# Kernel optimization log

Hardware: AMD Instinct MI355X
Metric: run time of the kernel (lower is better)

The kernel has to match this reference:

```python
import jax, jax.numpy as jnp
import numpy as np

N_NODES = 50000
N_EDGES = 1600000
IN_FEATS = 256
NUM_HEADS = 4
OUT_FEATS = 32
NEG_SLOPE = 0.2


def setup_inputs() -> dict:
    key = jax.random.key(0)
    k_feat, k_src, k_dst, k_w, k_al, k_ar = jax.random.split(key, 6)
    feat = jax.random.normal(k_feat, (N_NODES, IN_FEATS), dtype=jnp.float32)
    src = jax.random.randint(k_src, (N_EDGES,), 0, N_NODES, dtype=jnp.int32)
    dst = jax.random.randint(k_dst, (N_EDGES,), 0, N_NODES, dtype=jnp.int32)
    # Glorot/xavier-like scales
    w_scale = np.sqrt(2.0 / (IN_FEATS + NUM_HEADS * OUT_FEATS)).astype(np.float32)
    a_scale = np.sqrt(2.0 / (1 + OUT_FEATS)).astype(np.float32)
    W_fc = jax.random.normal(k_w, (NUM_HEADS * OUT_FEATS, IN_FEATS), dtype=jnp.float32) * w_scale
    attn_l = jax.random.normal(k_al, (1, NUM_HEADS, OUT_FEATS), dtype=jnp.float32) * a_scale
    attn_r = jax.random.normal(k_ar, (1, NUM_HEADS, OUT_FEATS), dtype=jnp.float32) * a_scale
    bias = jnp.zeros((NUM_HEADS * OUT_FEATS,), dtype=jnp.float32)
    return {"feat": feat, "W_fc": W_fc, "attn_l": attn_l, "attn_r": attn_r,
            "bias": bias, "src": src, "dst": dst}


def reference(feat, W_fc, attn_l, attn_r, bias, src, dst):
    N = feat.shape[0]
    H, F = NUM_HEADS, OUT_FEATS
    # dense projection: [N, H, F]
    h = (feat @ W_fc.T).reshape(N, H, F)
    # per-node attention logits: [N, H]
    el = (h * attn_l).sum(axis=-1)
    er = (h * attn_r).sum(axis=-1)
    # u_add_v edge score + leaky relu: [E, H]
    e = el[src] + er[dst]
    e = jnp.where(e >= 0, e, NEG_SLOPE * e)
    # segment softmax over destination nodes
    m = jax.ops.segment_max(e, dst, num_segments=N)          # [N, H]
    m = jnp.where(jnp.isfinite(m), m, 0.0)                   # guard 0-in-degree
    e_exp = jnp.exp(e - m[dst])                              # [E, H]
    denom = jax.ops.segment_sum(e_exp, dst, num_segments=N)  # [N, H]
    denom = jnp.where(denom > 0, denom, 1.0)
    a = e_exp / denom[dst]                                   # [E, H]
    # weighted message aggregation: [N, H, F]
    msg = h[src] * a[:, :, None]                             # [E, H, F]
    out = jax.ops.segment_sum(msg, dst, num_segments=N)
    out = out + bias.reshape(1, H, F)
    return out
```

## Files before the change

kernel.cpp:

```cpp
#include <hip/hip_runtime.h>

typedef __attribute__((ext_vector_type(8))) short bf16x8;
typedef __attribute__((ext_vector_type(4))) float f32x4;

#define IN_F 256
#define HF 128
#define NHEADS 4
#define NEG 0.2f

#define RB 256
#define NBP 200
#define CHUNK 6400
#define ITPT 25
#define BCAP 10000

__device__ __forceinline__ unsigned short f2bf(float x) {
    unsigned u = __float_as_uint(x);
    unsigned r = (u + 0x7FFFu + ((u >> 16) & 1u)) >> 16;
    return (unsigned short)r;
}
__device__ __forceinline__ float bf2f(unsigned short b) {
    return __uint_as_float((unsigned)b << 16);
}

__global__ __launch_bounds__(256) void wconv_kernel(const float* __restrict__ W,
                                                    unsigned short* __restrict__ Wb) {
    int i = (blockIdx.x * 256 + threadIdx.x) * 4;
    if (i < HF * IN_F) {
        float4 v = *(const float4*)&W[i];
        ushort4 o;
        o.x = f2bf(v.x); o.y = f2bf(v.y); o.z = f2bf(v.z); o.w = f2bf(v.w);
        *(ushort4*)&Wb[i] = o;
    }
}

__global__ __launch_bounds__(256) void gemm_kernel(
    const float* __restrict__ feat, const unsigned short* __restrict__ Wb,
    const float* __restrict__ al, const float* __restrict__ ar,
    unsigned short* __restrict__ hb, float* __restrict__ el, float* __restrict__ er,
    int N)
{
    __shared__ char smem[64 * 256 * 2];
    const int t = threadIdx.x;
    const int lane = t & 63;
    const int wid = t >> 6;
    const int n0 = blockIdx.x * 64;
    const int lr = lane & 15;
    const int lkO = (lane >> 4) * 8;

    bf16x8 b[2][8];
#pragma unroll
    for (int nj = 0; nj < 2; nj++)
#pragma unroll
        for (int ks = 0; ks < 8; ks++)
            b[nj][ks] = *(const bf16x8*)&Wb[(size_t)(wid * 32 + nj * 16 + lr) * IN_F + ks * 32 + lkO];

    const float4 z4 = make_float4(0.f, 0.f, 0.f, 0.f);
#pragma unroll
    for (int i = 0; i < 16; i++) {
        int flat = i * 1024 + t * 4;
        int row = flat >> 8;
        int col = flat & 255;
        int n = n0 + row;
        float4 v = (n < N) ? *(const float4*)&feat[(size_t)n * IN_F + col] : z4;
        ushort4 s;
        s.x = f2bf(v.x); s.y = f2bf(v.y); s.z = f2bf(v.z); s.w = f2bf(v.w);
        int byte = (row * 512 + col * 2) ^ ((row & 7) << 4);
        *(ushort4*)(smem + byte) = s;
    }
    __syncthreads();

    f32x4 acc[4][2];
#pragma unroll
    for (int mi = 0; mi < 4; mi++)
#pragma unroll
        for (int nj = 0; nj < 2; nj++) acc[mi][nj] = (f32x4){0.f, 0.f, 0.f, 0.f};

#pragma unroll
    for (int mi = 0; mi < 4; mi++) {
        const int r = mi * 16 + lr;
#pragma unroll
        for (int ks = 0; ks < 8; ks++) {
            int byte = (r * 512 + (ks * 32 + lkO) * 2) ^ ((r & 7) << 4);
            bf16x8 a = *(const bf16x8*)(smem + byte);
            acc[mi][0] = __builtin_amdgcn_mfma_f32_16x16x32_bf16(a, b[0][ks], acc[mi][0], 0, 0, 0);
            acc[mi][1] = __builtin_amdgcn_mfma_f32_16x16x32_bf16(a, b[1][ks], acc[mi][1], 0, 0, 0);
        }
    }

    float alc0 = al[wid * 32 + lr],      arc0 = ar[wid * 32 + lr];
    float alc1 = al[wid * 32 + 16 + lr], arc1 = ar[wid * 32 + 16 + lr];
    const int crow = (lane >> 4) * 4;
#pragma unroll
    for (int mi = 0; mi < 4; mi++)
#pragma unroll
        for (int j = 0; j < 4; j++) {
            int n = n0 + mi * 16 + crow + j;
            if (n < N) {
                hb[(size_t)n * HF + wid * 32 + lr]      = f2bf(acc[mi][0][j]);
                hb[(size_t)n * HF + wid * 32 + 16 + lr] = f2bf(acc[mi][1][j]);
            }
            float e = acc[mi][0][j] * alc0 + acc[mi][1][j] * alc1;
            float r2 = acc[mi][0][j] * arc0 + acc[mi][1][j] * arc1;
#pragma unroll
            for (int off = 1; off < 16; off <<= 1) {
                e += __shfl_xor(e, off);
                r2 += __shfl_xor(r2, off);
            }
            if (lr == 0 && n < N) {
                el[n * 4 + wid] = e;
                er[n * 4 + wid] = r2;
            }
        }
}

__global__ __launch_bounds__(256) void part_kernel(const int* __restrict__ src,
                                                   const int* __restrict__ dst,
                                                   int* __restrict__ ebuf,
                                                   int* __restrict__ cntArr,
                                                   int* __restrict__ ofsArr, int E) {
    __shared__ int cnt[256];
    __shared__ int sc[256];
    __shared__ int cur[256];
    __shared__ int stage[CHUNK];
    const int blk = blockIdx.x, t = threadIdx.x;
    const int eb = blk * CHUNK;
    cnt[t] = 0;
    __syncthreads();

    int bkt[ITPT], ent[ITPT];
#pragma unroll
    for (int i = 0; i < ITPT; i++) {
        int idx = eb + i * 256 + t;
        int b = NBP - 1, e = 0;
        if (idx < E) {
            int d = dst[idx];
            int s = src[idx];
            b = d >> 8;
            e = s | ((d & 255) << 24);
        }
        bkt[i] = b;
        ent[i] = e;
        atomicAdd(&cnt[b], 1);
    }
    __syncthreads();
    int orig = cnt[t];
    sc[t] = orig;
    __syncthreads();
    for (int off = 1; off < 256; off <<= 1) {
        int v = (t >= off) ? sc[t - off] : 0;
        __syncthreads();
        sc[t] += v;
        __syncthreads();
    }
    int excl = sc[t] - orig;
    if (t < NBP) {
        cntArr[blk * NBP + t] = orig;
        ofsArr[blk * NBP + t] = excl;
    }
    cur[t] = excl;
    __syncthreads();
#pragma unroll
    for (int i = 0; i < ITPT; i++) {
        int pos = atomicAdd(&cur[bkt[i]], 1);
        stage[pos] = ent[i];
    }
    __syncthreads();
#pragma unroll
    for (int i = 0; i < ITPT; i++) {
        int idx = i * 256 + t;
        ebuf[eb + idx] = stage[idx];
    }
}

__global__ __launch_bounds__(256) void bscan_kernel(const int* __restrict__ cntArr,
                                                    int* __restrict__ bucketStart, int nblk) {
    __shared__ int sums[256];
    const int t = threadIdx.x;
    int s = 0;
    if (t < NBP)
        for (int blk = 0; blk < nblk; blk++) s += cntArr[blk * NBP + t];
    sums[t] = s;
    __syncthreads();
    for (int off = 1; off < 256; off <<= 1) {
        int v = (t >= off) ? sums[t - off] : 0;
        __syncthreads();
        sums[t] += v;
        __syncthreads();
    }
    if (t < NBP) bucketStart[t] = sums[t] - s;
}

__global__ __launch_bounds__(256) void bsort_kernel(const int* __restrict__ ebuf,
                                                    const int* __restrict__ cntArr,
                                                    const int* __restrict__ ofsArr,
                                                    const int* __restrict__ bucketStart,
                                                    int* __restrict__ rowStart,
                                                    int* __restrict__ esrc,
                                                    int nblk, int N, int E) {
    __shared__ int lcnt[256];
    __shared__ int lsc[256];
    __shared__ int lcur[256];
    __shared__ int sorted[BCAP];
    const int b = blockIdx.x, t = threadIdx.x;
    const int gbase = bucketStart[b];
    lcnt[t] = 0;
    __syncthreads();

    int rbase = 0, rlen = 0;
    if (t < nblk) {
        rbase = t * CHUNK + ofsArr[t * NBP + b];
        rlen = cntArr[t * NBP + b];
    }
    int i = 0;
    for (; i + 3 < rlen; i += 4) {
        unsigned e0 = (unsigned)ebuf[rbase + i];
        unsigned e1 = (unsigned)ebuf[rbase + i + 1];
        unsigned e2 = (unsigned)ebuf[rbase + i + 2];
        unsigned e3 = (unsigned)ebuf[rbase + i + 3];
        atomicAdd(&lcnt[e0 >> 24], 1);
        atomicAdd(&lcnt[e1 >> 24], 1);
        atomicAdd(&lcnt[e2 >> 24], 1);
        atomicAdd(&lcnt[e3 >> 24], 1);
    }
    for (; i < rlen; i++) {
        unsigned e = (unsigned)ebuf[rbase + i];
        atomicAdd(&lcnt[e >> 24], 1);
    }
    __syncthreads();
    int orig = lcnt[t];
    lsc[t] = orig;
    __syncthreads();
    for (int off = 1; off < 256; off <<= 1) {
        int v = (t >= off) ? lsc[t - off] : 0;
        __syncthreads();
        lsc[t] += v;
        __syncthreads();
    }
    int excl = lsc[t] - orig;
    int node = b * RB + t;
    if (node < N) rowStart[node] = gbase + excl;
    if (b == 0 && t == 0) rowStart[N] = E;
    lcur[t] = excl;
    __syncthreads();
    i = 0;
    for (; i + 3 < rlen; i += 4) {
        unsigned e0 = (unsigned)ebuf[rbase + i];
        unsigned e1 = (unsigned)ebuf[rbase + i + 1];
        unsigned e2 = (unsigned)ebuf[rbase + i + 2];
        unsigned e3 = (unsigned)ebuf[rbase + i + 3];
        sorted[atomicAdd(&lcur[e0 >> 24], 1)] = (int)(e0 & 0xFFFFFFu);
        sorted[atomicAdd(&lcur[e1 >> 24], 1)] = (int)(e1 & 0xFFFFFFu);
        sorted[atomicAdd(&lcur[e2 >> 24], 1)] = (int)(e2 & 0xFFFFFFu);
        sorted[atomicAdd(&lcur[e3 >> 24], 1)] = (int)(e3 & 0xFFFFFFu);
    }
    for (; i < rlen; i++) {
        unsigned e = (unsigned)ebuf[rbase + i];
        sorted[atomicAdd(&lcur[e >> 24], 1)] = (int)(e & 0xFFFFFFu);
    }
    __syncthreads();
    const int total = lsc[255];
    for (int k = t; k < total; k += 256) esrc[gbase + k] = sorted[k];
}

__global__ __launch_bounds__(256) void agg_kernel(const int* __restrict__ rowStart,
                                                  const int* __restrict__ esrc,
                                                  const unsigned short* __restrict__ hb,
                                                  const float* __restrict__ el,
                                                  const float* __restrict__ er,
                                                  const float* __restrict__ bias,
                                                  float* __restrict__ out, int N) {
    const int wid = threadIdx.x >> 6;
    const int lane = threadIdx.x & 63;
    const int n = blockIdx.x * 4 + wid;
    if (n >= N) return;
    const int lg = lane & 15;
    const int grp = lane >> 4;
    const int head = lg >> 2;
    const float ern = er[n * NHEADS + head];
    const int beg = rowStart[n];
    const int end = rowStart[n + 1];

    float acc[8];
#pragma unroll
    for (int i = 0; i < 8; i++) acc[i] = 0.f;
    float den = 0.f;

#pragma unroll 4
    for (int j = beg + grp; j < end; j += 4) {
        int s = esrc[j];
        float x = el[s * NHEADS + head] + ern;
        x = x >= 0.f ? x : NEG * x;
        float sv = __expf(x);
        uint4 hv = *(const uint4*)&hb[(size_t)s * HF + lg * 8];
        acc[0] += sv * bf2f((unsigned short)(hv.x & 0xFFFFu));
        acc[1] += sv * bf2f((unsigned short)(hv.x >> 16));
        acc[2] += sv * bf2f((unsigned short)(hv.y & 0xFFFFu));
        acc[3] += sv * bf2f((unsigned short)(hv.y >> 16));
        acc[4] += sv * bf2f((unsigned short)(hv.z & 0xFFFFu));
        acc[5] += sv * bf2f((unsigned short)(hv.z >> 16));
        acc[6] += sv * bf2f((unsigned short)(hv.w & 0xFFFFu));
        acc[7] += sv * bf2f((unsigned short)(hv.w >> 16));
        den += sv;
    }

#pragma unroll
    for (int off = 16; off < 64; off <<= 1) {
#pragma unroll
        for (int i = 0; i < 8; i++) acc[i] += __shfl_xor(acc[i], off);
        den += __shfl_xor(den, off);
    }

    if (lane < 16) {
        float inv = 1.f / (den > 0.f ? den : 1.f);
        float4 b0 = *(const float4*)&bias[lg * 8];
        float4 b1 = *(const float4*)&bias[lg * 8 + 4];
        float4 o0, o1;
        o0.x = acc[0] * inv + b0.x; o0.y = acc[1] * inv + b0.y;
        o0.z = acc[2] * inv + b0.z; o0.w = acc[3] * inv + b0.w;
        o1.x = acc[4] * inv + b1.x; o1.y = acc[5] * inv + b1.y;
        o1.z = acc[6] * inv + b1.z; o1.w = acc[7] * inv + b1.w;
        *(float4*)&out[(size_t)n * HF + lg * 8] = o0;
        *(float4*)&out[(size_t)n * HF + lg * 8 + 4] = o1;
    }
}

extern "C" void kernel_launch(void* const* d_in, const int* in_sizes, int n_in,
                              void* d_out, int out_size, void* d_ws, size_t ws_size,
                              hipStream_t stream) {
    const float* feat = (const float*)d_in[0];
    const float* W    = (const float*)d_in[1];
    const float* al   = (const float*)d_in[2];
    const float* ar   = (const float*)d_in[3];
    const float* bias = (const float*)d_in[4];
    const int*   src  = (const int*)d_in[5];
    const int*   dst  = (const int*)d_in[6];
    const int N = in_sizes[0] / IN_F;
    const int E = in_sizes[5];
    float* out = (float*)d_out;

    const int nblk = (E + CHUNK - 1) / CHUNK;
    const int NBUCK = (N + RB - 1) / RB;

    unsigned short* hb = (unsigned short*)d_ws;
    unsigned short* Wb = hb + (size_t)N * HF;
    float* el       = (float*)(Wb + HF * IN_F);
    float* er       = el + (size_t)N * NHEADS;
    int* rowStart   = (int*)(er + (size_t)N * NHEADS);
    int* esrc       = rowStart + (N + 1);
    int* ebuf       = esrc + E;
    int* cntArr     = ebuf + (size_t)nblk * CHUNK;
    int* ofsArr     = cntArr + (size_t)nblk * NBP;
    int* bucketStart= ofsArr + (size_t)nblk * NBP;

    wconv_kernel<<<(HF * IN_F / 4 + 255) / 256, 256, 0, stream>>>(W, Wb);
    part_kernel<<<nblk, 256, 0, stream>>>(src, dst, ebuf, cntArr, ofsArr, E);
    gemm_kernel<<<(N + 63) / 64, 256, 0, stream>>>(feat, Wb, al, ar, hb, el, er, N);
    bscan_kernel<<<1, 256, 0, stream>>>(cntArr, bucketStart, nblk);
    bsort_kernel<<<NBUCK, 256, 0, stream>>>(ebuf, cntArr, ofsArr, bucketStart,
                                            rowStart, esrc, nblk, N, E);
    agg_kernel<<<(N + 3) / 4, 256, 0, stream>>>(rowStart, esrc, hb, el, er, bias, out, N);
}
```

Measured before the change: 158.0 us.

## Merge GEMM and edge partition into one launch, fold scans into bsort

```diff
diff --git a/kernel.cpp b/kernel.cpp
--- a/kernel.cpp
+++ b/kernel.cpp
@@ -14,6 +14,8 @@
 #define ITPT 25
 #define BCAP 10000
 
+#define K1_SMEM 32768
+
 __device__ __forceinline__ unsigned short f2bf(float x) {
     unsigned u = __float_as_uint(x);
     unsigned r = (u + 0x7FFFu + ((u >> 16) & 1u)) >> 16;
@@ -22,190 +24,181 @@
 __device__ __forceinline__ float bf2f(unsigned short b) {
     return __uint_as_float((unsigned)b << 16);
 }
-
-__global__ __launch_bounds__(256) void wconv_kernel(const float* __restrict__ W,
-                                                    unsigned short* __restrict__ Wb) {
-    int i = (blockIdx.x * 256 + threadIdx.x) * 4;
-    if (i < HF * IN_F) {
-        float4 v = *(const float4*)&W[i];
-        ushort4 o;
-        o.x = f2bf(v.x); o.y = f2bf(v.y); o.z = f2bf(v.z); o.w = f2bf(v.w);
-        *(ushort4*)&Wb[i] = o;
-    }
-}
-
-__global__ __launch_bounds__(256) void gemm_kernel(
-    const float* __restrict__ feat, const unsigned short* __restrict__ Wb,
+__device__ __forceinline__ bf16x8 cvt8(float4 x, float4 y) {
+    bf16x8 r;
+    r[0] = f2bf(x.x); r[1] = f2bf(x.y); r[2] = f2bf(x.z); r[3] = f2bf(x.w);
+    r[4] = f2bf(y.x); r[5] = f2bf(y.y); r[6] = f2bf(y.z); r[7] = f2bf(y.w);
+    return r;
+}
+
+__global__ __launch_bounds__(256) void fused1_kernel(
+    const float* __restrict__ feat, const float* __restrict__ W,
     const float* __restrict__ al, const float* __restrict__ ar,
     unsigned short* __restrict__ hb, float* __restrict__ el, float* __restrict__ er,
-    int N)
+    const int* __restrict__ src, const int* __restrict__ dst,
+    int* __restrict__ ebuf, int* __restrict__ cntArr, int* __restrict__ ofsArr,
+    int N, int E, int GG)
 {
-    __shared__ char smem[64 * 256 * 2];
+    extern __shared__ char smem[];
     const int t = threadIdx.x;
-    const int lane = t & 63;
-    const int wid = t >> 6;
-    const int n0 = blockIdx.x * 64;
-    const int lr = lane & 15;
-    const int lkO = (lane >> 4) * 8;
-
-    bf16x8 b[2][8];
-#pragma unroll
-    for (int nj = 0; nj < 2; nj++)
-#pragma unroll
-        for (int ks = 0; ks < 8; ks++)
-            b[nj][ks] = *(const bf16x8*)&Wb[(size_t)(wid * 32 + nj * 16 + lr) * IN_F + ks * 32 + lkO];
-
-    const float4 z4 = make_float4(0.f, 0.f, 0.f, 0.f);
-#pragma unroll
-    for (int i = 0; i < 16; i++) {
-        int flat = i * 1024 + t * 4;
-        int row = flat >> 8;
-        int col = flat & 255;
-        int n = n0 + row;
-        float4 v = (n < N) ? *(const float4*)&feat[(size_t)n * IN_F + col] : z4;
-        ushort4 s;
-        s.x = f2bf(v.x); s.y = f2bf(v.y); s.z = f2bf(v.z); s.w = f2bf(v.w);
-        int byte = (row * 512 + col * 2) ^ ((row & 7) << 4);
-        *(ushort4*)(smem + byte) = s;
-    }
-    __syncthreads();
-
-    f32x4 acc[4][2];
-#pragma unroll
-    for (int mi = 0; mi < 4; mi++)
-#pragma unroll
-        for (int nj = 0; nj < 2; nj++) acc[mi][nj] = (f32x4){0.f, 0.f, 0.f, 0.f};
-
-#pragma unroll
-    for (int mi = 0; mi < 4; mi++) {
-        const int r = mi * 16 + lr;
-#pragma unroll
-        for (int ks = 0; ks < 8; ks++) {
-            int byte = (r * 512 + (ks * 32 + lkO) * 2) ^ ((r & 7) << 4);
-            bf16x8 a = *(const bf16x8*)(smem + byte);
-            acc[mi][0] = __builtin_amdgcn_mfma_f32_16x16x32_bf16(a, b[0][ks], acc[mi][0], 0, 0, 0);
-            acc[mi][1] = __builtin_amdgcn_mfma_f32_16x16x32_bf16(a, b[1][ks], acc[mi][1], 0, 0, 0);
-        }
-    }
-
-    float alc0 = al[wid * 32 + lr],      arc0 = ar[wid * 32 + lr];
-    float alc1 = al[wid * 32 + 16 + lr], arc1 = ar[wid * 32 + 16 + lr];
-    const int crow = (lane >> 4) * 4;
-#pragma unroll
-    for (int mi = 0; mi < 4; mi++)
-#pragma unroll
-        for (int j = 0; j < 4; j++) {
-            int n = n0 + mi * 16 + crow + j;
-            if (n < N) {
-                hb[(size_t)n * HF + wid * 32 + lr]      = f2bf(acc[mi][0][j]);
-                hb[(size_t)n * HF + wid * 32 + 16 + lr] = f2bf(acc[mi][1][j]);
+
+    if ((int)blockIdx.x < GG) {
+        const int lane = t & 63;
+        const int wid = t >> 6;
+        const int n0 = blockIdx.x * 64;
+        const int lr = lane & 15;
+        const int lkO = (lane >> 4) * 8;
+
+        bf16x8 b[2][8];
+#pragma unroll
+        for (int nj = 0; nj < 2; nj++)
+#pragma unroll
+            for (int ks = 0; ks < 8; ks++) {
+                const float* wrow = &W[(size_t)(wid * 32 + nj * 16 + lr) * IN_F + ks * 32 + lkO];
+                b[nj][ks] = cvt8(*(const float4*)wrow, *(const float4*)(wrow + 4));
             }
-            float e = acc[mi][0][j] * alc0 + acc[mi][1][j] * alc1;
-            float r2 = acc[mi][0][j] * arc0 + acc[mi][1][j] * arc1;
-#pragma unroll
-            for (int off = 1; off < 16; off <<= 1) {
-                e += __shfl_xor(e, off);
-                r2 += __shfl_xor(r2, off);
+
+        const float4 z4 = make_float4(0.f, 0.f, 0.f, 0.f);
+#pragma unroll
+        for (int i = 0; i < 16; i++) {
+            int flat = i * 1024 + t * 4;
+            int row = flat >> 8;
+            int col = flat & 255;
+            int n = n0 + row;
+            float4 v = (n < N) ? *(const float4*)&feat[(size_t)n * IN_F + col] : z4;
+            ushort4 s;
+            s.x = f2bf(v.x); s.y = f2bf(v.y); s.z = f2bf(v.z); s.w = f2bf(v.w);
+            int byte = (row * 512 + col * 2) ^ ((row & 7) << 4);
+            *(ushort4*)(smem + byte) = s;
+        }
+        __syncthreads();
+
+        f32x4 acc[4][2];
+#pragma unroll
+        for (int mi = 0; mi < 4; mi++)
+#pragma unroll
+            for (int nj = 0; nj < 2; nj++) acc[mi][nj] = (f32x4){0.f, 0.f, 0.f, 0.f};
+
+#pragma unroll
+        for (int mi = 0; mi < 4; mi++) {
+            const int r = mi * 16 + lr;
+#pragma unroll
+            for (int ks = 0; ks < 8; ks++) {
+                int byte = (r * 512 + (ks * 32 + lkO) * 2) ^ ((r & 7) << 4);
+                bf16x8 a = *(const bf16x8*)(smem + byte);
+                acc[mi][0] = __builtin_amdgcn_mfma_f32_16x16x32_bf16(a, b[0][ks], acc[mi][0], 0, 0, 0);
+                acc[mi][1] = __builtin_amdgcn_mfma_f32_16x16x32_bf16(a, b[1][ks], acc[mi][1], 0, 0, 0);
             }
-            if (lr == 0 && n < N) {
-                el[n * 4 + wid] = e;
-                er[n * 4 + wid] = r2;
+        }
+
+        float alc0 = al[wid * 32 + lr],      arc0 = ar[wid * 32 + lr];
+        float alc1 = al[wid * 32 + 16 + lr], arc1 = ar[wid * 32 + 16 + lr];
+        const int crow = (lane >> 4) * 4;
+#pragma unroll
+        for (int mi = 0; mi < 4; mi++)
+#pragma unroll
+            for (int j = 0; j < 4; j++) {
+                int n = n0 + mi * 16 + crow + j;
+                if (n < N) {
+                    hb[(size_t)n * HF + wid * 32 + lr]      = f2bf(acc[mi][0][j]);
+                    hb[(size_t)n * HF + wid * 32 + 16 + lr] = f2bf(acc[mi][1][j]);
+                }
+                float e = acc[mi][0][j] * alc0 + acc[mi][1][j] * alc1;
+                float r2 = acc[mi][0][j] * arc0 + acc[mi][1][j] * arc1;
+#pragma unroll
+                for (int off = 1; off < 16; off <<= 1) {
+                    e += __shfl_xor(e, off);
+                    r2 += __shfl_xor(r2, off);
+                }
+                if (lr == 0 && n < N) {
+                    el[n * 4 + wid] = e;
+                    er[n * 4 + wid] = r2;
+                }
             }
-        }
-}
-
-__global__ __launch_bounds__(256) void part_kernel(const int* __restrict__ src,
-                                                   const int* __restrict__ dst,
-                                                   int* __restrict__ ebuf,
-                                                   int* __restrict__ cntArr,
-                                                   int* __restrict__ ofsArr, int E) {
-    __shared__ int cnt[256];
-    __shared__ int sc[256];
-    __shared__ int cur[256];
-    __shared__ int stage[CHUNK];
-    const int blk = blockIdx.x, t = threadIdx.x;
-    const int eb = blk * CHUNK;
-    cnt[t] = 0;
-    __syncthreads();
-
-    int bkt[ITPT], ent[ITPT];
-#pragma unroll
-    for (int i = 0; i < ITPT; i++) {
-        int idx = eb + i * 256 + t;
-        int b = NBP - 1, e = 0;
-        if (idx < E) {
-            int d = dst[idx];
-            int s = src[idx];
-            b = d >> 8;
-            e = s | ((d & 255) << 24);
-        }
-        bkt[i] = b;
-        ent[i] = e;
-        atomicAdd(&cnt[b], 1);
-    }
-    __syncthreads();
-    int orig = cnt[t];
-    sc[t] = orig;
-    __syncthreads();
-    for (int off = 1; off < 256; off <<= 1) {
-        int v = (t >= off) ? sc[t - off] : 0;
-        __syncthreads();
-        sc[t] += v;
-        __syncthreads();
-    }
-    int excl = sc[t] - orig;
-    if (t < NBP) {
-        cntArr[blk * NBP + t] = orig;
-        ofsArr[blk * NBP + t] = excl;
-    }
-    cur[t] = excl;
-    __syncthreads();
-#pragma unroll
-    for (int i = 0; i < ITPT; i++) {
-        int pos = atomicAdd(&cur[bkt[i]], 1);
-        stage[pos] = ent[i];
-    }
-    __syncthreads();
-#pragma unroll
-    for (int i = 0; i < ITPT; i++) {
-        int idx = i * 256 + t;
-        ebuf[eb + idx] = stage[idx];
-    }
-}
-
-__global__ __launch_bounds__(256) void bscan_kernel(const int* __restrict__ cntArr,
-                                                    int* __restrict__ bucketStart, int nblk) {
-    __shared__ int sums[256];
-    const int t = threadIdx.x;
-    int s = 0;
-    if (t < NBP)
-        for (int blk = 0; blk < nblk; blk++) s += cntArr[blk * NBP + t];
-    sums[t] = s;
-    __syncthreads();
-    for (int off = 1; off < 256; off <<= 1) {
-        int v = (t >= off) ? sums[t - off] : 0;
-        __syncthreads();
-        sums[t] += v;
-        __syncthreads();
-    }
-    if (t < NBP) bucketStart[t] = sums[t] - s;
+    } else {
+        int* cnt = (int*)smem;
+        int* sc  = cnt + 256;
+        int* cur = sc + 256;
+        int* stage = cur + 256;
+        const int blk = blockIdx.x - GG;
+        const int eb = blk * CHUNK;
+        cnt[t] = 0;
+        __syncthreads();
+
+        int bkt[ITPT], ent[ITPT];
+#pragma unroll
+        for (int i = 0; i < ITPT; i++) {
+            int idx = eb + i * 256 + t;
+            int b = NBP - 1, e = 0;
+            if (idx < E) {
+                int d = dst[idx];
+                int s = src[idx];
+                b = d >> 8;
+                e = s | ((d & 255) << 24);
+            }
+            bkt[i] = b;
+            ent[i] = e;
+            atomicAdd(&cnt[b], 1);
+        }
+        __syncthreads();
+        int orig = cnt[t];
+        sc[t] = orig;
+        __syncthreads();
+        for (int off = 1; off < 256; off <<= 1) {
+            int v = (t >= off) ? sc[t - off] : 0;
+            __syncthreads();
+            sc[t] += v;
+            __syncthreads();
+        }
+        int excl = sc[t] - orig;
+        if (t < NBP) {
+            cntArr[blk * NBP + t] = orig;
+            ofsArr[blk * NBP + t] = excl;
+        }
+        cur[t] = excl;
+        __syncthreads();
+#pragma unroll
+        for (int i = 0; i < ITPT; i++) {
+            int pos = atomicAdd(&cur[bkt[i]], 1);
+            stage[pos] = ent[i];
+        }
+        __syncthreads();
+#pragma unroll
+        for (int i = 0; i < ITPT; i++) {
+            int idx = i * 256 + t;
+            ebuf[eb + idx] = stage[idx];
+        }
+    }
 }
 
 __global__ __launch_bounds__(256) void bsort_kernel(const int* __restrict__ ebuf,
                                                     const int* __restrict__ cntArr,
                                                     const int* __restrict__ ofsArr,
-                                                    const int* __restrict__ bucketStart,
                                                     int* __restrict__ rowStart,
                                                     int* __restrict__ esrc,
                                                     int nblk, int N, int E) {
     __shared__ int lcnt[256];
     __shared__ int lsc[256];
     __shared__ int lcur[256];
+    __shared__ int gbase_sh;
     __shared__ int sorted[BCAP];
     const int b = blockIdx.x, t = threadIdx.x;
-    const int gbase = bucketStart[b];
+
+    int tot = 0;
+    if (t < NBP)
+        for (int blk = 0; blk < nblk; blk++) tot += cntArr[blk * NBP + t];
+    lsc[t] = tot;
+    __syncthreads();
+    for (int off = 1; off < 256; off <<= 1) {
+        int v = (t >= off) ? lsc[t - off] : 0;
+        __syncthreads();
+        lsc[t] += v;
+        __syncthreads();
+    }
+    if (t == b) gbase_sh = lsc[t] - tot;
     lcnt[t] = 0;
     __syncthreads();
+    const int gbase = gbase_sh;
 
     int rbase = 0, rlen = 0;
     if (t < nblk) {
@@ -341,23 +334,19 @@
 
     const int nblk = (E + CHUNK - 1) / CHUNK;
     const int NBUCK = (N + RB - 1) / RB;
+    const int GG = (N + 63) / 64;
 
     unsigned short* hb = (unsigned short*)d_ws;
-    unsigned short* Wb = hb + (size_t)N * HF;
-    float* el       = (float*)(Wb + HF * IN_F);
+    float* el       = (float*)(hb + (size_t)N * HF);
     float* er       = el + (size_t)N * NHEADS;
     int* rowStart   = (int*)(er + (size_t)N * NHEADS);
     int* esrc       = rowStart + (N + 1);
     int* ebuf       = esrc + E;
     int* cntArr     = ebuf + (size_t)nblk * CHUNK;
     int* ofsArr     = cntArr + (size_t)nblk * NBP;
-    int* bucketStart= ofsArr + (size_t)nblk * NBP;
-
-    wconv_kernel<<<(HF * IN_F / 4 + 255) / 256, 256, 0, stream>>>(W, Wb);
-    part_kernel<<<nblk, 256, 0, stream>>>(src, dst, ebuf, cntArr, ofsArr, E);
-    gemm_kernel<<<(N + 63) / 64, 256, 0, stream>>>(feat, Wb, al, ar, hb, el, er, N);
-    bscan_kernel<<<1, 256, 0, stream>>>(cntArr, bucketStart, nblk);
-    bsort_kernel<<<NBUCK, 256, 0, stream>>>(ebuf, cntArr, ofsArr, bucketStart,
-                                            rowStart, esrc, nblk, N, E);
+
+    fused1_kernel<<<GG + nblk, 256, K1_SMEM, stream>>>(
+        feat, W, al, ar, hb, el, er, src, dst, ebuf, cntArr, ofsArr, N, E, GG);
+    bsort_kernel<<<NBUCK, 256, 0, stream>>>(ebuf, cntArr, ofsArr, rowStart, esrc, nblk, N, E);
     agg_kernel<<<(N + 3) / 4, 256, 0, stream>>>(rowStart, esrc, hb, el, er, bias, out, N);
 }
```

Result: faster. 153.4 us (-2.9%).
